# Kernel tuning notes

Measured on AMD Instinct MI355X. Metric: run time of the kernel, lower is better.

## Reference

```python
import jax, jax.numpy as jnp
import numpy as np

N = 10000
E = 160000
D_IN = 512
D_OUT = 512


def setup_inputs() -> dict:
    key = jax.random.key(0)
    k1, k2, k3, k4, k5 = jax.random.split(key, 5)
    x = jax.random.normal(k1, (N, D_IN), dtype=jnp.float32)
    edge_index = jax.random.randint(k2, (2, E), 0, N, dtype=jnp.int64)
    edge_attr = jax.random.uniform(k3, (E,), dtype=jnp.float32)
    W = jax.random.normal(k4, (D_IN, D_OUT), dtype=jnp.float32) * 0.05
    b = jax.random.normal(k5, (D_OUT,), dtype=jnp.float32) * 0.05
    return {"x": x, "edge_index": edge_index, "edge_attr": edge_attr, "W": W, "b": b}


def reference(x, edge_index, edge_attr, W, b):
    # PyG GCNConv with normalize=True, add_self_loops=True, edge_weight=edge_attr.
    n = x.shape[0]
    row, col = edge_index[0], edge_index[1]
    # Add self loops with weight 1.0 (fill_value=1.)
    loop = jnp.arange(n, dtype=edge_index.dtype)
    row_f = jnp.concatenate([row, loop])      # [E+N] source nodes
    col_f = jnp.concatenate([col, loop])      # [E+N] target nodes
    ew = jnp.concatenate([edge_attr, jnp.ones((n,), dtype=edge_attr.dtype)])
    # Symmetric normalization: deg computed over target index (col)
    deg = jax.ops.segment_sum(ew, col_f, num_segments=n)
    dinv = jnp.where(deg > 0, jax.lax.rsqrt(deg), 0.0)
    norm = dinv[row_f] * ew * dinv[col_f]     # [E+N]
    # Linear transform (no bias inside lin), then gather-scale-scatter
    h = x @ W                                  # [N, D_OUT]
    msg = h[row_f] * norm[:, None]             # [E+N, D_OUT]
    out = jax.ops.segment_sum(msg, col_f, num_segments=n)
    return out + b
```

## Files before the change

kernel.cpp:

```cpp
#include <hip/hip_runtime.h>

#define NN 10000
#define EE 160000
#define DD 512
#define CAP 128

typedef float floatx4 __attribute__((ext_vector_type(4)));
typedef short short8 __attribute__((ext_vector_type(8)));

#define AS3(p) ((__attribute__((address_space(3))) void*)(p))
#define AS1(p) ((const __attribute__((address_space(1))) void*)(p))

static __device__ __forceinline__ unsigned short f2bf(float f) {
    unsigned int u = __float_as_uint(f);
    unsigned int r = (u + 0x7fffu + ((u >> 16) & 1u)) >> 16;
    return (unsigned short)r;
}
static __device__ __forceinline__ float bflo(unsigned int u) {
    return __uint_as_float(u << 16);
}
static __device__ __forceinline__ float bfhi(unsigned int u) {
    return __uint_as_float(u & 0xffff0000u);
}


#define XB_BLOCKS 5000
#define WT_BLOCKS 256
#define EDGE_BLOCKS 625

__global__ __launch_bounds__(256) void k_prep(const float* __restrict__ x,
                                              const float* __restrict__ W,
                                              const int* __restrict__ row,
                                              const int* __restrict__ col,
                                              const float* __restrict__ ew,
                                              unsigned short* __restrict__ xb,
                                              unsigned short* __restrict__ wtb,
                                              float* __restrict__ deg,
                                              int* __restrict__ cursor,
                                              uint2* __restrict__ erw) {
    const int b = blockIdx.x;
    const int tid = threadIdx.x;
    if (b < XB_BLOCKS) {
        int gid = b * 256 + tid;
        float4 v = *(const float4*)&x[(size_t)gid * 4];
        unsigned int p0 = (unsigned int)f2bf(v.x) | ((unsigned int)f2bf(v.y) << 16);
        unsigned int p1 = (unsigned int)f2bf(v.z) | ((unsigned int)f2bf(v.w) << 16);
        *(uint2*)&xb[(size_t)gid * 4] = make_uint2(p0, p1);
    } else if (b < XB_BLOCKS + WT_BLOCKS) {
        __shared__ float T[32][33];
        int idx = b - XB_BLOCKS;
        int bi = idx & 15;
        int bj = idx >> 4;
        int r0 = tid >> 5;
        int cc = tid & 31;
        #pragma unroll
        for (int k = 0; k < 4; k++) {
            int r = r0 + k * 8;
            T[r][cc] = W[(size_t)(bi * 32 + r) * DD + bj * 32 + cc];
        }
        __syncthreads();
        #pragma unroll
        for (int k = 0; k < 4; k++) {
            int r = r0 + k * 8;
            wtb[(size_t)(bj * 32 + r) * DD + bi * 32 + cc] = f2bf(T[cc][r]);
        }
    } else {
        int e = (b - XB_BLOCKS - WT_BLOCKS) * 256 + tid;
        int r = row[e];
        int t = col[e];
        float w = ew[e];
        atomicAdd(&deg[t], w);
        int p = atomicAdd(&cursor[t], 1);
        if (p < CAP) erw[t * CAP + p] = make_uint2((unsigned int)r, __float_as_uint(w));
    }
}


__global__ __launch_bounds__(256) void k_gemm_mfma(const unsigned short* __restrict__ xb,
                                                   const unsigned short* __restrict__ wtb,
                                                   const float* __restrict__ deg,
                                                   unsigned short* __restrict__ hb) {
    __shared__ unsigned short As[64 * 32];
    __shared__ unsigned short Bs[128 * 32];

    const int tid = threadIdx.x;
    const int wave = tid >> 6;
    const int lane = tid & 63;

    const int bm = blockIdx.x * 64;
    const int bn = blockIdx.y * 128;

    const int wm = (wave >> 1) * 32;
    const int wn = (wave & 1) * 64;

    const int fm = lane & 15;
    const int kb = (lane >> 4) * 8;

    floatx4 acc[2][4];
    #pragma unroll
    for (int i = 0; i < 2; i++)
        #pragma unroll
        for (int j = 0; j < 4; j++)
            acc[i][j] = (floatx4){0.f, 0.f, 0.f, 0.f};

    const int srow = lane >> 2;
    const int scol = (lane & 3) * 8;

    for (int k0 = 0; k0 < DD; k0 += 32) {
        {
            int r = wave * 16 + srow;
            int gr = bm + r; if (gr > NN - 1) gr = NN - 1;
            __builtin_amdgcn_global_load_lds(AS1(xb + (size_t)gr * DD + k0 + scol),
                                             AS3(&As[wave * 512]), 16, 0, 0);
        }
        #pragma unroll
        for (int cc = 0; cc < 2; cc++) {
            int c = wave + cc * 4;
            int nr = bn + c * 16 + srow;
            __builtin_amdgcn_global_load_lds(AS1(wtb + (size_t)nr * DD + k0 + scol),
                                             AS3(&Bs[c * 512]), 16, 0, 0);
        }
        __syncthreads();

        short8 af[2], bfr[4];
        #pragma unroll
        for (int mi = 0; mi < 2; mi++)
            af[mi] = *(const short8*)&As[(wm + mi * 16 + fm) * 32 + kb];
        #pragma unroll
        for (int ni = 0; ni < 4; ni++)
            bfr[ni] = *(const short8*)&Bs[(wn + ni * 16 + fm) * 32 + kb];

        #pragma unroll
        for (int mi = 0; mi < 2; mi++)
            #pragma unroll
            for (int ni = 0; ni < 4; ni++)
                acc[mi][ni] = __builtin_amdgcn_mfma_f32_16x16x32_bf16(af[mi], bfr[ni], acc[mi][ni], 0, 0, 0);

        __syncthreads();
    }

    float dv[2][4];
    #pragma unroll
    for (int mi = 0; mi < 2; mi++) {
        int rbase = bm + wm + mi * 16 + (lane >> 4) * 4;
        #pragma unroll
        for (int j = 0; j < 4; j++) {
            int rg = rbase + j; if (rg > NN - 1) rg = NN - 1;
            dv[mi][j] = rsqrtf(deg[rg] + 1.0f);
        }
    }

    #pragma unroll
    for (int mi = 0; mi < 2; mi++) {
        #pragma unroll
        for (int ni = 0; ni < 4; ni++) {
            int colg = bn + wn + ni * 16 + (lane & 15);
            int rbase = bm + wm + mi * 16 + (lane >> 4) * 4;
            #pragma unroll
            for (int j = 0; j < 4; j++) {
                int rg = rbase + j;
                if (rg < NN) hb[(size_t)rg * DD + colg] = f2bf(acc[mi][ni][j] * dv[mi][j]);
            }
        }
    }
}


#define EDGE_FMA(P, W) \
    acc[0] += bflo(P.x) * W; acc[1] += bfhi(P.x) * W; \
    acc[2] += bflo(P.y) * W; acc[3] += bfhi(P.y) * W; \
    acc[4] += bflo(P.z) * W; acc[5] += bfhi(P.z) * W; \
    acc[6] += bflo(P.w) * W; acc[7] += bfhi(P.w) * W;

__global__ __launch_bounds__(128) void k_aggregate(const int* __restrict__ cursor,
                                                   const uint2* __restrict__ erw,
                                                   const unsigned short* __restrict__ hb,
                                                   const float* __restrict__ deg,
                                                   const float* __restrict__ bias,
                                                   float* __restrict__ out) {
    const int h = threadIdx.x >> 6;
    const int t = threadIdx.x & 63;
    const int i = blockIdx.x * 2 + h;
    const int c = t << 3;

    __shared__ int   s_r[2][CAP];
    __shared__ float s_w[2][CAP];

    int cnt = cursor[i];
    if (cnt > CAP) cnt = CAP;
    const uint2* bkt = erw + (size_t)i * CAP;
    if (t < cnt)      { uint2 p = bkt[t];      s_r[h][t]      = (int)p.x; s_w[h][t]      = __uint_as_float(p.y); }
    if (t + 64 < cnt) { uint2 p = bkt[t + 64]; s_r[h][t + 64] = (int)p.x; s_w[h][t + 64] = __uint_as_float(p.y); }

    float dv = rsqrtf(deg[i] + 1.0f);
    uint4 hv = *(const uint4*)&hb[(size_t)i * DD + c];
    float4 bv0 = *(const float4*)&bias[c];
    float4 bv1 = *(const float4*)&bias[c + 4];

    __syncthreads();

    float acc[8] = {0.f, 0.f, 0.f, 0.f, 0.f, 0.f, 0.f, 0.f};

    int j = 0;
    for (; j + 4 <= cnt; j += 4) {
        int r0 = s_r[h][j];     float w0 = s_w[h][j];
        int r1 = s_r[h][j + 1]; float w1 = s_w[h][j + 1];
        int r2 = s_r[h][j + 2]; float w2 = s_w[h][j + 2];
        int r3 = s_r[h][j + 3]; float w3 = s_w[h][j + 3];
        uint4 p0 = *(const uint4*)&hb[(size_t)r0 * DD + c];
        uint4 p1 = *(const uint4*)&hb[(size_t)r1 * DD + c];
        uint4 p2 = *(const uint4*)&hb[(size_t)r2 * DD + c];
        uint4 p3 = *(const uint4*)&hb[(size_t)r3 * DD + c];
        EDGE_FMA(p0, w0)
        EDGE_FMA(p1, w1)
        EDGE_FMA(p2, w2)
        EDGE_FMA(p3, w3)
    }
    for (; j < cnt; j++) {
        int r0 = s_r[h][j]; float w0 = s_w[h][j];
        uint4 p0 = *(const uint4*)&hb[(size_t)r0 * DD + c];
        EDGE_FMA(p0, w0)
    }

    float4 o0, o1;
    o0.x = (acc[0] + bflo(hv.x)) * dv + bv0.x;
    o0.y = (acc[1] + bfhi(hv.x)) * dv + bv0.y;
    o0.z = (acc[2] + bflo(hv.y)) * dv + bv0.z;
    o0.w = (acc[3] + bfhi(hv.y)) * dv + bv0.w;
    o1.x = (acc[4] + bflo(hv.z)) * dv + bv1.x;
    o1.y = (acc[5] + bfhi(hv.z)) * dv + bv1.y;
    o1.z = (acc[6] + bflo(hv.w)) * dv + bv1.z;
    o1.w = (acc[7] + bfhi(hv.w)) * dv + bv1.w;
    *(float4*)&out[(size_t)i * DD + c] = o0;
    *(float4*)&out[(size_t)i * DD + c + 4] = o1;
}

extern "C" void kernel_launch(void* const* d_in, const int* in_sizes, int n_in,
                              void* d_out, int out_size, void* d_ws, size_t ws_size,
                              hipStream_t stream) {
    const float* x  = (const float*)d_in[0];
    const int*   ei = (const int*)d_in[1];
    const float* ea = (const float*)d_in[2];
    const float* W  = (const float*)d_in[3];
    const float* b  = (const float*)d_in[4];
    float* out = (float*)d_out;

    char* ws = (char*)d_ws;
    unsigned short* hb   = (unsigned short*)ws;
    unsigned short* xb   = (unsigned short*)(ws + 10240000);
    unsigned short* wtb  = (unsigned short*)(ws + 20480000);
    float* deg    = (float*)(ws + 21004288);
    int*   cursor = (int*)  (ws + 21045248);
    uint2* erw    = (uint2*)(ws + 21086208);

    const int* row = ei;
    const int* col = ei + EE;

    hipMemsetAsync(deg, 0, 81920, stream);

    k_prep<<<XB_BLOCKS + WT_BLOCKS + EDGE_BLOCKS, 256, 0, stream>>>(x, W, row, col, ea,
                                                                    xb, wtb, deg, cursor, erw);

    dim3 ggrid((NN + 63) / 64, DD / 128);
    k_gemm_mfma<<<ggrid, 256, 0, stream>>>(xb, wtb, deg, hb);

    k_aggregate<<<NN / 2, 128, 0, stream>>>(cursor, erw, hb, deg, b, out);
}
```

Before: 137.1 us.

## Fuse x-to-bf16 conversion into GEMM A-tile load; deepen aggregate unroll

Drops the separate pass that converts x to bf16 in the prep kernel. The GEMM now reads fp32 x directly, converts it in registers and stores bf16 into the LDS A tile, which removes a 20MB write plus re-read round trip. The trade-off is that the A-tile load becomes a synchronous register path instead of an async global_load_lds, and each x row is re-read for each of the 4 N-tile blocks. The aggregate kernel also unrolls the gather to 8 edges at a time and adds an occupancy hint to launch_bounds.

```diff
diff --git a/kernel.cpp b/kernel.cpp
--- a/kernel.cpp
+++ b/kernel.cpp
@@ -16,6 +16,9 @@
     unsigned int r = (u + 0x7fffu + ((u >> 16) & 1u)) >> 16;
     return (unsigned short)r;
 }
+static __device__ __forceinline__ unsigned int pack2bf(float a, float b) {
+    return (unsigned int)f2bf(a) | ((unsigned int)f2bf(b) << 16);
+}
 static __device__ __forceinline__ float bflo(unsigned int u) {
     return __uint_as_float(u << 16);
 }
@@ -24,33 +27,23 @@
 }
 
 
-#define XB_BLOCKS 5000
 #define WT_BLOCKS 256
 #define EDGE_BLOCKS 625
 
-__global__ __launch_bounds__(256) void k_prep(const float* __restrict__ x,
-                                              const float* __restrict__ W,
+__global__ __launch_bounds__(256) void k_prep(const float* __restrict__ W,
                                               const int* __restrict__ row,
                                               const int* __restrict__ col,
                                               const float* __restrict__ ew,
-                                              unsigned short* __restrict__ xb,
                                               unsigned short* __restrict__ wtb,
                                               float* __restrict__ deg,
                                               int* __restrict__ cursor,
                                               uint2* __restrict__ erw) {
     const int b = blockIdx.x;
     const int tid = threadIdx.x;
-    if (b < XB_BLOCKS) {
-        int gid = b * 256 + tid;
-        float4 v = *(const float4*)&x[(size_t)gid * 4];
-        unsigned int p0 = (unsigned int)f2bf(v.x) | ((unsigned int)f2bf(v.y) << 16);
-        unsigned int p1 = (unsigned int)f2bf(v.z) | ((unsigned int)f2bf(v.w) << 16);
-        *(uint2*)&xb[(size_t)gid * 4] = make_uint2(p0, p1);
-    } else if (b < XB_BLOCKS + WT_BLOCKS) {
+    if (b < WT_BLOCKS) {
         __shared__ float T[32][33];
-        int idx = b - XB_BLOCKS;
-        int bi = idx & 15;
-        int bj = idx >> 4;
+        int bi = b & 15;
+        int bj = b >> 4;
         int r0 = tid >> 5;
         int cc = tid & 31;
         #pragma unroll
@@ -65,7 +58,7 @@
             wtb[(size_t)(bj * 32 + r) * DD + bi * 32 + cc] = f2bf(T[cc][r]);
         }
     } else {
-        int e = (b - XB_BLOCKS - WT_BLOCKS) * 256 + tid;
+        int e = (b - WT_BLOCKS) * 256 + tid;
         int r = row[e];
         int t = col[e];
         float w = ew[e];
@@ -76,7 +69,7 @@
 }
 
 
-__global__ __launch_bounds__(256) void k_gemm_mfma(const unsigned short* __restrict__ xb,
+__global__ __launch_bounds__(256) void k_gemm_mfma(const float* __restrict__ x,
                                                    const unsigned short* __restrict__ wtb,
                                                    const float* __restrict__ deg,
                                                    unsigned short* __restrict__ hb) {
@@ -103,22 +96,31 @@
         for (int j = 0; j < 4; j++)
             acc[i][j] = (floatx4){0.f, 0.f, 0.f, 0.f};
 
+    const int ar = tid >> 2;
+    const int acg = (tid & 3) * 8;
+    int agr = bm + ar; if (agr > NN - 1) agr = NN - 1;
+
     const int srow = lane >> 2;
     const int scol = (lane & 3) * 8;
 
     for (int k0 = 0; k0 < DD; k0 += 32) {
-        {
-            int r = wave * 16 + srow;
-            int gr = bm + r; if (gr > NN - 1) gr = NN - 1;
-            __builtin_amdgcn_global_load_lds(AS1(xb + (size_t)gr * DD + k0 + scol),
-                                             AS3(&As[wave * 512]), 16, 0, 0);
-        }
         #pragma unroll
         for (int cc = 0; cc < 2; cc++) {
             int c = wave + cc * 4;
             int nr = bn + c * 16 + srow;
             __builtin_amdgcn_global_load_lds(AS1(wtb + (size_t)nr * DD + k0 + scol),
                                              AS3(&Bs[c * 512]), 16, 0, 0);
+        }
+        {
+            const float* src = x + (size_t)agr * DD + k0 + acg;
+            float4 v0 = *(const float4*)src;
+            float4 v1 = *(const float4*)(src + 4);
+            uint4 pk;
+            pk.x = pack2bf(v0.x, v0.y);
+            pk.y = pack2bf(v0.z, v0.w);
+            pk.z = pack2bf(v1.x, v1.y);
+            pk.w = pack2bf(v1.z, v1.w);
+            *(uint4*)&As[ar * 32 + acg] = pk;
         }
         __syncthreads();
 
@@ -172,12 +174,12 @@
     acc[4] += bflo(P.z) * W; acc[5] += bfhi(P.z) * W; \
     acc[6] += bflo(P.w) * W; acc[7] += bfhi(P.w) * W;
 
-__global__ __launch_bounds__(128) void k_aggregate(const int* __restrict__ cursor,
-                                                   const uint2* __restrict__ erw,
-                                                   const unsigned short* __restrict__ hb,
-                                                   const float* __restrict__ deg,
-                                                   const float* __restrict__ bias,
-                                                   float* __restrict__ out) {
+__global__ __launch_bounds__(128, 8) void k_aggregate(const int* __restrict__ cursor,
+                                                      const uint2* __restrict__ erw,
+                                                      const unsigned short* __restrict__ hb,
+                                                      const float* __restrict__ deg,
+                                                      const float* __restrict__ bias,
+                                                      float* __restrict__ out) {
     const int h = threadIdx.x >> 6;
     const int t = threadIdx.x & 63;
     const int i = blockIdx.x * 2 + h;
@@ -202,23 +204,31 @@
     float acc[8] = {0.f, 0.f, 0.f, 0.f, 0.f, 0.f, 0.f, 0.f};
 
     int j = 0;
+    for (; j + 8 <= cnt; j += 8) {
+        uint4 p0 = *(const uint4*)&hb[(size_t)s_r[h][j    ] * DD + c];
+        uint4 p1 = *(const uint4*)&hb[(size_t)s_r[h][j + 1] * DD + c];
+        uint4 p2 = *(const uint4*)&hb[(size_t)s_r[h][j + 2] * DD + c];
+        uint4 p3 = *(const uint4*)&hb[(size_t)s_r[h][j + 3] * DD + c];
+        uint4 p4 = *(const uint4*)&hb[(size_t)s_r[h][j + 4] * DD + c];
+        uint4 p5 = *(const uint4*)&hb[(size_t)s_r[h][j + 5] * DD + c];
+        uint4 p6 = *(const uint4*)&hb[(size_t)s_r[h][j + 6] * DD + c];
+        uint4 p7 = *(const uint4*)&hb[(size_t)s_r[h][j + 7] * DD + c];
+        float w0 = s_w[h][j],     w1 = s_w[h][j + 1], w2 = s_w[h][j + 2], w3 = s_w[h][j + 3];
+        float w4 = s_w[h][j + 4], w5 = s_w[h][j + 5], w6 = s_w[h][j + 6], w7 = s_w[h][j + 7];
+        EDGE_FMA(p0, w0) EDGE_FMA(p1, w1) EDGE_FMA(p2, w2) EDGE_FMA(p3, w3)
+        EDGE_FMA(p4, w4) EDGE_FMA(p5, w5) EDGE_FMA(p6, w6) EDGE_FMA(p7, w7)
+    }
     for (; j + 4 <= cnt; j += 4) {
-        int r0 = s_r[h][j];     float w0 = s_w[h][j];
-        int r1 = s_r[h][j + 1]; float w1 = s_w[h][j + 1];
-        int r2 = s_r[h][j + 2]; float w2 = s_w[h][j + 2];
-        int r3 = s_r[h][j + 3]; float w3 = s_w[h][j + 3];
-        uint4 p0 = *(const uint4*)&hb[(size_t)r0 * DD + c];
-        uint4 p1 = *(const uint4*)&hb[(size_t)r1 * DD + c];
-        uint4 p2 = *(const uint4*)&hb[(size_t)r2 * DD + c];
-        uint4 p3 = *(const uint4*)&hb[(size_t)r3 * DD + c];
-        EDGE_FMA(p0, w0)
-        EDGE_FMA(p1, w1)
-        EDGE_FMA(p2, w2)
-        EDGE_FMA(p3, w3)
+        uint4 p0 = *(const uint4*)&hb[(size_t)s_r[h][j    ] * DD + c];
+        uint4 p1 = *(const uint4*)&hb[(size_t)s_r[h][j + 1] * DD + c];
+        uint4 p2 = *(const uint4*)&hb[(size_t)s_r[h][j + 2] * DD + c];
+        uint4 p3 = *(const uint4*)&hb[(size_t)s_r[h][j + 3] * DD + c];
+        float w0 = s_w[h][j], w1 = s_w[h][j + 1], w2 = s_w[h][j + 2], w3 = s_w[h][j + 3];
+        EDGE_FMA(p0, w0) EDGE_FMA(p1, w1) EDGE_FMA(p2, w2) EDGE_FMA(p3, w3)
     }
     for (; j < cnt; j++) {
-        int r0 = s_r[h][j]; float w0 = s_w[h][j];
-        uint4 p0 = *(const uint4*)&hb[(size_t)r0 * DD + c];
+        uint4 p0 = *(const uint4*)&hb[(size_t)s_r[h][j] * DD + c];
+        float w0 = s_w[h][j];
         EDGE_FMA(p0, w0)
     }
 
@@ -247,22 +257,20 @@
 
     char* ws = (char*)d_ws;
     unsigned short* hb   = (unsigned short*)ws;
-    unsigned short* xb   = (unsigned short*)(ws + 10240000);
-    unsigned short* wtb  = (unsigned short*)(ws + 20480000);
-    float* deg    = (float*)(ws + 21004288);
-    int*   cursor = (int*)  (ws + 21045248);
-    uint2* erw    = (uint2*)(ws + 21086208);
+    unsigned short* wtb  = (unsigned short*)(ws + 10240000);
+    float* deg    = (float*)(ws + 10764288);
+    int*   cursor = (int*)  (ws + 10805248);
+    uint2* erw    = (uint2*)(ws + 10846208);
 
     const int* row = ei;
     const int* col = ei + EE;
 
     hipMemsetAsync(deg, 0, 81920, stream);
 
-    k_prep<<<XB_BLOCKS + WT_BLOCKS + EDGE_BLOCKS, 256, 0, stream>>>(x, W, row, col, ea,
-                                                                    xb, wtb, deg, cursor, erw);
+    k_prep<<<WT_BLOCKS + EDGE_BLOCKS, 256, 0, stream>>>(W, row, col, ea, wtb, deg, cursor, erw);
 
     dim3 ggrid((NN + 63) / 64, DD / 128);
-    k_gemm_mfma<<<ggrid, 256, 0, stream>>>(xb, wtb, deg, hb);
+    k_gemm_mfma<<<ggrid, 256, 0, stream>>>(x, wtb, deg, hb);
 
     k_aggregate<<<NN / 2, 128, 0, stream>>>(cursor, erw, hb, deg, b, out);
 }
```

Result: slower. 161.0 us (+17.4%).

## Split aggregate columns across two blocks with narrower per-thread loads

Applied to the files above, without the earlier changes.

The aggregation kernel now launches twice as many blocks, each covering half of the 512 output columns, so each thread handles 4 columns with 8-byte loads instead of 8 columns with 16-byte loads. The main loop unrolls to 8 edges so more gathers are in flight, and launch bounds request higher occupancy. The aim is more parallelism and better latency hiding for the irregular row gathers. In exchange, edge-list loading into shared memory and the degree reads are duplicated per half, and the narrower loads issue more memory instructions per byte.

```diff
diff --git a/kernel.cpp b/kernel.cpp
--- a/kernel.cpp
+++ b/kernel.cpp
@@ -166,22 +166,22 @@
 }
 
 
-#define EDGE_FMA(P, W) \
+#define EDGE_FMA2(P, W) \
     acc[0] += bflo(P.x) * W; acc[1] += bfhi(P.x) * W; \
-    acc[2] += bflo(P.y) * W; acc[3] += bfhi(P.y) * W; \
-    acc[4] += bflo(P.z) * W; acc[5] += bfhi(P.z) * W; \
-    acc[6] += bflo(P.w) * W; acc[7] += bfhi(P.w) * W;
-
-__global__ __launch_bounds__(128) void k_aggregate(const int* __restrict__ cursor,
-                                                   const uint2* __restrict__ erw,
-                                                   const unsigned short* __restrict__ hb,
-                                                   const float* __restrict__ deg,
-                                                   const float* __restrict__ bias,
-                                                   float* __restrict__ out) {
+    acc[2] += bflo(P.y) * W; acc[3] += bfhi(P.y) * W;
+
+__global__ __launch_bounds__(128, 8) void k_aggregate(const int* __restrict__ cursor,
+                                                      const uint2* __restrict__ erw,
+                                                      const unsigned short* __restrict__ hb,
+                                                      const float* __restrict__ deg,
+                                                      const float* __restrict__ bias,
+                                                      float* __restrict__ out) {
     const int h = threadIdx.x >> 6;
     const int t = threadIdx.x & 63;
-    const int i = blockIdx.x * 2 + h;
-    const int c = t << 3;
+    const int bid = blockIdx.x;
+    const int half = bid & 1;
+    const int i = (bid >> 1) * 2 + h;
+    const int c = half * 256 + t * 4;
 
     __shared__ int   s_r[2][CAP];
     __shared__ float s_w[2][CAP];
@@ -193,46 +193,48 @@
     if (t + 64 < cnt) { uint2 p = bkt[t + 64]; s_r[h][t + 64] = (int)p.x; s_w[h][t + 64] = __uint_as_float(p.y); }
 
     float dv = rsqrtf(deg[i] + 1.0f);
-    uint4 hv = *(const uint4*)&hb[(size_t)i * DD + c];
-    float4 bv0 = *(const float4*)&bias[c];
-    float4 bv1 = *(const float4*)&bias[c + 4];
+    uint2 hv = *(const uint2*)&hb[(size_t)i * DD + c];
+    float4 bv = *(const float4*)&bias[c];
 
     __syncthreads();
 
-    float acc[8] = {0.f, 0.f, 0.f, 0.f, 0.f, 0.f, 0.f, 0.f};
+    float acc[4] = {0.f, 0.f, 0.f, 0.f};
 
     int j = 0;
+    for (; j + 8 <= cnt; j += 8) {
+        uint2 p0 = *(const uint2*)&hb[(size_t)s_r[h][j    ] * DD + c];
+        uint2 p1 = *(const uint2*)&hb[(size_t)s_r[h][j + 1] * DD + c];
+        uint2 p2 = *(const uint2*)&hb[(size_t)s_r[h][j + 2] * DD + c];
+        uint2 p3 = *(const uint2*)&hb[(size_t)s_r[h][j + 3] * DD + c];
+        uint2 p4 = *(const uint2*)&hb[(size_t)s_r[h][j + 4] * DD + c];
+        uint2 p5 = *(const uint2*)&hb[(size_t)s_r[h][j + 5] * DD + c];
+        uint2 p6 = *(const uint2*)&hb[(size_t)s_r[h][j + 6] * DD + c];
+        uint2 p7 = *(const uint2*)&hb[(size_t)s_r[h][j + 7] * DD + c];
+        float w0 = s_w[h][j],     w1 = s_w[h][j + 1], w2 = s_w[h][j + 2], w3 = s_w[h][j + 3];
+        float w4 = s_w[h][j + 4], w5 = s_w[h][j + 5], w6 = s_w[h][j + 6], w7 = s_w[h][j + 7];
+        EDGE_FMA2(p0, w0) EDGE_FMA2(p1, w1) EDGE_FMA2(p2, w2) EDGE_FMA2(p3, w3)
+        EDGE_FMA2(p4, w4) EDGE_FMA2(p5, w5) EDGE_FMA2(p6, w6) EDGE_FMA2(p7, w7)
+    }
     for (; j + 4 <= cnt; j += 4) {
-        int r0 = s_r[h][j];     float w0 = s_w[h][j];
-        int r1 = s_r[h][j + 1]; float w1 = s_w[h][j + 1];
-        int r2 = s_r[h][j + 2]; float w2 = s_w[h][j + 2];
-        int r3 = s_r[h][j + 3]; float w3 = s_w[h][j + 3];
-        uint4 p0 = *(const uint4*)&hb[(size_t)r0 * DD + c];
-        uint4 p1 = *(const uint4*)&hb[(size_t)r1 * DD + c];
-        uint4 p2 = *(const uint4*)&hb[(size_t)r2 * DD + c];
-        uint4 p3 = *(const uint4*)&hb[(size_t)r3 * DD + c];
-        EDGE_FMA(p0, w0)
-        EDGE_FMA(p1, w1)
-        EDGE_FMA(p2, w2)
-        EDGE_FMA(p3, w3)
+        uint2 p0 = *(const uint2*)&hb[(size_t)s_r[h][j    ] * DD + c];
+        uint2 p1 = *(const uint2*)&hb[(size_t)s_r[h][j + 1] * DD + c];
+        uint2 p2 = *(const uint2*)&hb[(size_t)s_r[h][j + 2] * DD + c];
+        uint2 p3 = *(const uint2*)&hb[(size_t)s_r[h][j + 3] * DD + c];
+        float w0 = s_w[h][j], w1 = s_w[h][j + 1], w2 = s_w[h][j + 2], w3 = s_w[h][j + 3];
+        EDGE_FMA2(p0, w0) EDGE_FMA2(p1, w1) EDGE_FMA2(p2, w2) EDGE_FMA2(p3, w3)
     }
     for (; j < cnt; j++) {
-        int r0 = s_r[h][j]; float w0 = s_w[h][j];
-        uint4 p0 = *(const uint4*)&hb[(size_t)r0 * DD + c];
-        EDGE_FMA(p0, w0)
-    }
-
-    float4 o0, o1;
-    o0.x = (acc[0] + bflo(hv.x)) * dv + bv0.x;
-    o0.y = (acc[1] + bfhi(hv.x)) * dv + bv0.y;
-    o0.z = (acc[2] + bflo(hv.y)) * dv + bv0.z;
-    o0.w = (acc[3] + bfhi(hv.y)) * dv + bv0.w;
-    o1.x = (acc[4] + bflo(hv.z)) * dv + bv1.x;
-    o1.y = (acc[5] + bfhi(hv.z)) * dv + bv1.y;
-    o1.z = (acc[6] + bflo(hv.w)) * dv + bv1.z;
-    o1.w = (acc[7] + bfhi(hv.w)) * dv + bv1.w;
-    *(float4*)&out[(size_t)i * DD + c] = o0;
-    *(float4*)&out[(size_t)i * DD + c + 4] = o1;
+        uint2 p0 = *(const uint2*)&hb[(size_t)s_r[h][j] * DD + c];
+        float w0 = s_w[h][j];
+        EDGE_FMA2(p0, w0)
+    }
+
+    float4 o;
+    o.x = (acc[0] + bflo(hv.x)) * dv + bv.x;
+    o.y = (acc[1] + bfhi(hv.x)) * dv + bv.y;
+    o.z = (acc[2] + bflo(hv.y)) * dv + bv.z;
+    o.w = (acc[3] + bfhi(hv.y)) * dv + bv.w;
+    *(float4*)&out[(size_t)i * DD + c] = o;
 }
 
 extern "C" void kernel_launch(void* const* d_in, const int* in_sizes, int n_in,
@@ -264,5 +266,5 @@
     dim3 ggrid((NN + 63) / 64, DD / 128);
     k_gemm_mfma<<<ggrid, 256, 0, stream>>>(xb, wtb, deg, hb);
 
-    k_aggregate<<<NN / 2, 128, 0, stream>>>(cursor, erw, hb, deg, b, out);
-}
+    k_aggregate<<<NN, 128, 0, stream>>>(cursor, erw, hb, deg, b, out);
+}
```

New measurement: 132.9 us. 1.03x faster.
